# Kernel optimization log

Hardware: AMD Instinct MI355X
Metric: run time of the kernel (lower is better)

The kernel has to match this reference:

```python
import jax, jax.numpy as jnp
import numpy as np

NUM_HEADS = 16
QKV_FEATURES = 2048
HEAD_DIM = QKV_FEATURES // NUM_HEADS
THETA = 10000.0


def compute_freqs_cis(dim, length, start_pos=0, theta=THETA, dtype=jnp.float32):
    freqs = 1.0 / theta ** (jnp.arange(0, dim, 2, dtype=jnp.float32) / dim)
    t = jnp.arange(length, dtype=jnp.float32) + start_pos
    freqs = jnp.outer(t, freqs)  # (L, dim//2)
    return jnp.sin(freqs).astype(dtype), jnp.cos(freqs).astype(dtype)


def apply_rotary_emb(x, sin, cos):
    # x: (B, L, H, D); sin/cos: (L, D//2); interleaved-pair rotation
    x1 = x[..., 0::2]
    x2 = x[..., 1::2]
    sin = sin[None, :, None, :]
    cos = cos[None, :, None, :]
    y1 = x1 * cos - x2 * sin
    y2 = x1 * sin + x2 * cos
    return jnp.stack([y1, y2], axis=-1).reshape(x.shape)


def setup_inputs() -> dict:
    key = jax.random.key(0)
    ks = jax.random.split(key, 6)
    B, L, E = 2, 2048, 2048
    s_in = 1.0 / np.sqrt(E)
    s_out = 1.0 / np.sqrt(QKV_FEATURES)
    return {
        "x": jax.random.normal(ks[0], (B, L, E), jnp.float32),
        "Wq": jax.random.normal(ks[1], (E, QKV_FEATURES), jnp.float32) * s_in,
        "Wk": jax.random.normal(ks[2], (E, QKV_FEATURES), jnp.float32) * s_in,
        "Wv": jax.random.normal(ks[3], (E, QKV_FEATURES), jnp.float32) * s_in,
        "Wo": jax.random.normal(ks[4], (QKV_FEATURES, E), jnp.float32) * s_out,
        "bo": jnp.zeros((E,), jnp.float32),
    }


def reference(x, Wq, Wk, Wv, Wo, bo):
    B, L, E = x.shape
    H, D = NUM_HEADS, HEAD_DIM

    q = (x @ Wq).reshape(B, L, H, D)
    k = (x @ Wk).reshape(B, L, H, D)
    v = (x @ Wv).reshape(B, L, H, D)

    sin, cos = compute_freqs_cis(D, L)
    q = apply_rotary_emb(q, sin, cos)
    k = apply_rotary_emb(k, sin, cos)

    scale = D ** (-0.5)
    sim = jnp.einsum("bqhd,bkhd->bhqk", q, k) * scale

    pos = jnp.arange(L)
    causal_mask = pos[None, :] <= pos[:, None]  # (Lq, Lk)
    sim = jnp.where(causal_mask[None, None, :, :], sim, -1e9)

    attn = jax.nn.softmax(sim, axis=-1)
    out = jnp.einsum("bhqk,bkhd->bqhd", attn, v).reshape(B, L, H * D)
    return out @ Wo + bo
```

## Files before the change

kernel.cpp:

```cpp
#include <hip/hip_runtime.h>
#include <hip/hip_bf16.h>
#include <stdint.h>
#include <stddef.h>

#define B_   2
#define L_   2048
#define E_   2048
#define H_   16
#define D_   128
#define F_   2048
#define NROW (B_*L_)
#define QS   6144

typedef __bf16 bf16_t;
typedef __bf16 bf16x4 __attribute__((ext_vector_type(4)));
typedef __bf16 bf16x8 __attribute__((ext_vector_type(8)));
typedef float  f32x4  __attribute__((ext_vector_type(4)));

__device__ __forceinline__ void gload16(const void* g, void* l) {
  __builtin_amdgcn_global_load_lds(
      (const __attribute__((address_space(1))) void*)g,
      (__attribute__((address_space(3))) void*)l, 16, 0, 0);
}

#define VMC(n)  asm volatile("s_waitcnt vmcnt(" #n ")" ::: "memory")

__global__ __launch_bounds__(256) void k_convert(const float* __restrict__ in,
                                                 bf16_t* __restrict__ out, int n4) {
  int i = blockIdx.x*256 + threadIdx.x;
  if (i >= n4) return;
  float4 v = ((const float4*)in)[i];
  bf16x4 t;
  t[0] = (__bf16)v.x; t[1] = (__bf16)v.y; t[2] = (__bf16)v.z; t[3] = (__bf16)v.w;
  ((bf16x4*)out)[i] = t;
}

__global__ __launch_bounds__(256) void k_transpose_w4(const float* __restrict__ Wq,
                                                      const float* __restrict__ Wk,
                                                      const float* __restrict__ Wv,
                                                      const float* __restrict__ Wo,
                                                      bf16_t* __restrict__ wqkvt,
                                                      bf16_t* __restrict__ wot) {
  __shared__ float tile[32][33];
  const int z = blockIdx.z;
  const float* in = (z == 0) ? Wq : (z == 1) ? Wk : (z == 2) ? Wv : Wo;
  bf16_t* out = (z < 3) ? wqkvt + (size_t)z*F_*E_ : wot;
  const int ct = blockIdx.x, rt = blockIdx.y;
  const int c = threadIdx.x & 31, r0 = threadIdx.x >> 5;
  #pragma unroll
  for (int k = 0; k < 4; k++) {
    int r = r0 + k*8;
    tile[r][c] = in[(size_t)(rt*32 + r)*2048 + ct*32 + c];
  }
  __syncthreads();
  #pragma unroll
  for (int k = 0; k < 4; k++) {
    int r = r0 + k*8;
    out[(size_t)(ct*32 + r)*2048 + rt*32 + c] = (__bf16)tile[c][r];
  }
}

__global__ __launch_bounds__(256) void k_sincos(float2* __restrict__ sc) {
  int id = blockIdx.x*256 + threadIdx.x;
  int t = id >> 6, i = id & 63;
  float freq = powf(10000.0f, -(float)i / 64.0f);
  float a = (float)t * freq;
  sc[id] = make_float2(cosf(a), sinf(a));
}

__global__ __launch_bounds__(256) void k_rope2(bf16_t* __restrict__ qkv,
                                               const float2* __restrict__ sc,
                                               float qscale, int half) {
  int i = blockIdx.x*256 + threadIdx.x;
  const int part = (i >= half);
  int j = part ? i - half : i;
  int e  = j << 2;
  int d  = e & (F_-1);
  int ii = (d & (D_-1)) >> 1;
  int r  = e >> 11;
  int t  = r & (L_-1);
  bf16_t* p = qkv + (size_t)r*QS + part*F_ + d;
  const float scale = part ? 1.0f : qscale;
  bf16x4 v = *(const bf16x4*)p;
  float2 cs0 = sc[t*64 + ii];
  float2 cs1 = sc[t*64 + ii + 1];
  cs0.x *= scale; cs0.y *= scale; cs1.x *= scale; cs1.y *= scale;
  float x0 = (float)v[0], x1 = (float)v[1], x2 = (float)v[2], x3 = (float)v[3];
  bf16x4 o;
  o[0] = (__bf16)(x0*cs0.x - x1*cs0.y);
  o[1] = (__bf16)(x0*cs0.y + x1*cs0.x);
  o[2] = (__bf16)(x2*cs1.x - x3*cs1.y);
  o[3] = (__bf16)(x2*cs1.y + x3*cs1.x);
  *(bf16x4*)p = o;
}

__global__ __launch_bounds__(256) void k_transpose_v(const bf16_t* __restrict__ in,
                                                     bf16_t* __restrict__ out) {
  __shared__ bf16_t tile[32][33];
  const int lt = blockIdx.x, dt = blockIdx.y, bh = blockIdx.z;
  const int b = bh >> 4;
  const int h = bh & 15;
  const int c = threadIdx.x & 31, r0 = threadIdx.x >> 5;
  #pragma unroll
  for (int k = 0; k < 4; k++) {
    int r = r0 + k*8;
    tile[r][c] = in[(size_t)(b*L_ + lt*32 + r)*QS + h*D_ + dt*32 + c];
  }
  __syncthreads();
  #pragma unroll
  for (int k = 0; k < 4; k++) {
    int r = r0 + k*8;
    out[(size_t)(bh*D_ + dt*32 + r)*L_ + lt*32 + c] = tile[c][r];
  }
}

template<typename OutT, bool BIAS>
__global__ __launch_bounds__(256, 3) void k_gemm_bt(const bf16_t* __restrict__ A,
                                                    const bf16_t* __restrict__ BT,
                                                    OutT* __restrict__ C,
                                                    const float* __restrict__ bias,
                                                    int M, int N, int K) {
  __shared__ char sm[49152];
  const int tid = threadIdx.x, lane = tid & 63, wave = tid >> 6;
  const int wr = wave >> 1, wc = wave & 1;
  const int lr = lane & 15, lg = lane >> 4;
  const int nbx = N >> 7, nwg = nbx * (M >> 7);
  int bid = blockIdx.x;
  const int cpx = nwg >> 3;
  bid = (bid & 7)*cpx + (bid >> 3);
  const int bx = bid % nbx, by = bid / nbx;
  const int row0 = by << 7, col0 = bx << 7;
  const int sr  = tid >> 2;
  const int sxe = (((tid & 3) ^ ((sr >> 1) & 3)) << 3);
  const bf16_t* Ag = A  + (size_t)(row0 + sr)*K + sxe;
  const bf16_t* Bg = BT + (size_t)(col0 + sr)*K + sxe;
  const int dst0 = wave*1024;
  auto stage = [&](int t) {
    char* base = sm + (t % 3)*16384;
    const bf16_t* a = Ag + t*32;
    const bf16_t* b = Bg + t*32;
    gload16(a,                base + dst0);
    gload16(a + (size_t)64*K, base + 4096  + dst0);
    gload16(b,                base + 8192  + dst0);
    gload16(b + (size_t)64*K, base + 12288 + dst0);
  };
  const int cs   = (lg ^ ((lr >> 1) & 3)) << 4;
  const int arow = (wr*64 + lr)*64;
  const int brow = 8192 + (wc*64 + lr)*64;
  f32x4 acc[4][4] = {};
  stage(0); stage(1);
  const int nt = K >> 5;
  for (int t = 0; t < nt; t++) {
    if (t + 2 < nt)      { stage(t + 2); VMC(8); }
    else if (t + 1 < nt) { VMC(4); }
    else                 { VMC(0); }
    __builtin_amdgcn_s_barrier();
    const char* base = sm + (t % 3)*16384;
    bf16x8 af[4], bb[4];
    #pragma unroll
    for (int m = 0; m < 4; m++) af[m] = *(const bf16x8*)(base + arow + m*1024 + cs);
    #pragma unroll
    for (int n = 0; n < 4; n++) bb[n] = *(const bf16x8*)(base + brow + n*1024 + cs);
    asm volatile("s_waitcnt lgkmcnt(0)" ::: "memory");
    __builtin_amdgcn_sched_barrier(0);
    __builtin_amdgcn_s_setprio(1);
    #pragma unroll
    for (int m = 0; m < 4; m++)
      #pragma unroll
      for (int n = 0; n < 4; n++)
        acc[m][n] = __builtin_amdgcn_mfma_f32_16x16x32_bf16(af[m], bb[n], acc[m][n], 0, 0, 0);
    __builtin_amdgcn_s_setprio(0);
    __builtin_amdgcn_s_barrier();
  }
  #pragma unroll
  for (int m = 0; m < 4; m++) {
    #pragma unroll
    for (int n = 0; n < 4; n++) {
      const int col = col0 + wc*64 + n*16 + lr;
      const float bv = BIAS ? bias[col] : 0.0f;
      #pragma unroll
      for (int j = 0; j < 4; j++) {
        const int row = row0 + wr*64 + m*16 + lg*4 + j;
        C[(size_t)row*N + col] = (OutT)(acc[m][n][j] + bv);
      }
    }
  }
}

template<bool MASK>
__device__ __forceinline__ void attn_tile(
    int kv0, int wq0, int lr, int lg,
    const char* __restrict__ Kb, const char* __restrict__ Vb, char* __restrict__ Pb,
    const bf16x8 (&aq)[4], f32x4 (&o)[8], float& mrow, float& lsum) {
  const int swz = (lr & 7) << 4;
  f32x4 s[4] = {};
  #pragma unroll
  for (int kd = 0; kd < 4; kd++) {
    bf16x8 ak[4];
    #pragma unroll
    for (int n = 0; n < 4; n++)
      ak[n] = *(const bf16x8*)(Kb + (n*16 + lr)*256 + (((kd*4 + lg) << 4) ^ swz));
    __builtin_amdgcn_s_setprio(1);
    #pragma unroll
    for (int n = 0; n < 4; n++)
      s[n] = __builtin_amdgcn_mfma_f32_16x16x32_bf16(ak[n], aq[kd], s[n], 0, 0, 0);
    __builtin_amdgcn_s_setprio(0);
  }
  if (MASK) {
    const int q = wq0 + lr;
    #pragma unroll
    for (int n = 0; n < 4; n++)
      #pragma unroll
      for (int j = 0; j < 4; j++)
        if (kv0 + n*16 + lg*4 + j > q) s[n][j] = -30000.0f;
  }
  float pmax = fmaxf(
      fmaxf(fmaxf(fmaxf(s[0][0], s[0][1]), fmaxf(s[0][2], s[0][3])),
            fmaxf(fmaxf(s[1][0], s[1][1]), fmaxf(s[1][2], s[1][3]))),
      fmaxf(fmaxf(fmaxf(s[2][0], s[2][1]), fmaxf(s[2][2], s[2][3])),
            fmaxf(fmaxf(s[3][0], s[3][1]), fmaxf(s[3][2], s[3][3]))));
  pmax = fmaxf(pmax, __shfl_xor(pmax, 16));
  pmax = fmaxf(pmax, __shfl_xor(pmax, 32));
  if (!__all(pmax - mrow <= 8.0f)) {
    const float mnew = fmaxf(mrow, pmax);
    const float corr = exp2f(mrow - mnew);
    mrow = mnew;
    lsum *= corr;
    #pragma unroll
    for (int n2 = 0; n2 < 8; n2++) o[n2] *= corr;
  }
  float rs = 0.0f;
  #pragma unroll
  for (int n = 0; n < 4; n++)
    #pragma unroll
    for (int j = 0; j < 4; j++) {
      float p = exp2f(s[n][j] - mrow);
      s[n][j] = p;
      rs += p;
    }
  rs += __shfl_xor(rs, 16);
  rs += __shfl_xor(rs, 32);
  lsum += rs;
  #pragma unroll
  for (int n = 0; n < 4; n++) {
    bf16x4 pw;
    pw[0] = (__bf16)s[n][0]; pw[1] = (__bf16)s[n][1];
    pw[2] = (__bf16)s[n][2]; pw[3] = (__bf16)s[n][3];
    *(bf16x4*)(Pb + ((lr*128 + n*32 + lg*8) ^ swz)) = pw;
  }
  #pragma unroll
  for (int ks = 0; ks < 2; ks++) {
    bf16x8 pb = *(const bf16x8*)(Pb + ((lr*128 + ks*64 + lg*16) ^ swz));
    __builtin_amdgcn_s_setprio(1);
    #pragma unroll
    for (int n2 = 0; n2 < 8; n2++) {
      bf16x8 av = *(const bf16x8*)(Vb + (n2*16 + lr)*128 + (((ks*4 + lg) << 4) ^ swz));
      o[n2] = __builtin_amdgcn_mfma_f32_16x16x32_bf16(av, pb, o[n2], 0, 0, 0);
    }
    __builtin_amdgcn_s_setprio(0);
  }
}

__global__ __launch_bounds__(512, 4) void k_attn(const bf16_t* __restrict__ QKV,
                                                 const bf16_t* __restrict__ Vt,
                                                 bf16_t* __restrict__ O) {
  __shared__ bf16_t Ks[2][64*128];
  __shared__ bf16_t Vs[2][128*64];
  __shared__ bf16_t Pl[8][16*64];
  const int tid = threadIdx.x, lane = tid & 63, wave = tid >> 6;
  const int qt = (int)gridDim.x - 1 - (int)blockIdx.x;
  const int h = blockIdx.y, b = blockIdx.z;
  const int wq0 = qt*128 + wave*16;
  const int lr = lane & 15, lg = lane >> 4;
  char* Pb = (char*)&Pl[wave][0];
  const bf16_t* Q = QKV;
  const bf16_t* K = QKV + F_;

  bf16x8 aq[4];
  #pragma unroll
  for (int kd = 0; kd < 4; kd++)
    aq[kd] = *(const bf16x8*)&Q[(size_t)(b*L_ + wq0 + lr)*QS + h*D_ + kd*32 + lg*8];

  const int kr = tid >> 4, kc = tid & 15;
  const bf16_t* Kg0 = K + (size_t)(b*L_ + kr)*QS + h*D_ + ((kc ^ (kr & 7)) << 3);
  const int vr = tid >> 3, vc = tid & 7;
  const bf16_t* Vg0 = Vt + (size_t)((b*H_ + h)*D_ + vr)*L_ + ((vc ^ (vr & 7)) << 3);

  f32x4 o[8] = {};
  float mrow = -3.0e38f, lsum = 0.0f;
  const int ntb   = 2*qt + 2;
  const int nfull = (wq0 + 1) >> 6;
  const int nmine = ((wq0 + 15) >> 6) + 1;

  {
    char* kb = (char*)&Ks[0][0] + wave*1024;
    char* vb = (char*)&Vs[0][0] + wave*1024;
    gload16(Kg0,                 kb);
    gload16(Kg0 + (size_t)32*QS, kb + 8192);
    gload16(Vg0,                 vb);
    gload16(Vg0 + (size_t)64*L_, vb + 8192);
  }
  __syncthreads();

  int buf = 0;
  for (int t = 0; t < ntb; t++) {
    if (t + 1 < ntb) {
      const int kn = (t+1)*64;
      char* kb = (char*)&Ks[buf^1][0] + wave*1024;
      char* vb = (char*)&Vs[buf^1][0] + wave*1024;
      const bf16_t* kg = Kg0 + (size_t)kn*QS;
      const bf16_t* vg = Vg0 + kn;
      gload16(kg,                 kb);
      gload16(kg + (size_t)32*QS, kb + 8192);
      gload16(vg,                 vb);
      gload16(vg + (size_t)64*L_, vb + 8192);
    }
    const char* Kb = (const char*)&Ks[buf][0];
    const char* Vb = (const char*)&Vs[buf][0];
    if (t < nfull)
      attn_tile<false>(t*64, wq0, lr, lg, Kb, Vb, Pb, aq, o, mrow, lsum);
    else if (t < nmine)
      attn_tile<true >(t*64, wq0, lr, lg, Kb, Vb, Pb, aq, o, mrow, lsum);
    __syncthreads();
    buf ^= 1;
  }
  const float inv = 1.0f / lsum;
  bf16_t* orow = O + (size_t)(b*L_ + wq0 + lr)*F_ + h*D_ + lg*4;
  #pragma unroll
  for (int n2 = 0; n2 < 8; n2++) {
    bf16x4 ov;
    ov[0] = (__bf16)(o[n2][0]*inv); ov[1] = (__bf16)(o[n2][1]*inv);
    ov[2] = (__bf16)(o[n2][2]*inv); ov[3] = (__bf16)(o[n2][3]*inv);
    *(bf16x4*)(orow + n2*16) = ov;
  }
}

extern "C" void kernel_launch(void* const* d_in, const int* in_sizes, int n_in,
                              void* d_out, int out_size, void* d_ws, size_t ws_size,
                              hipStream_t stream) {
  const float* x  = (const float*)d_in[0];
  const float* Wq = (const float*)d_in[1];
  const float* Wk = (const float*)d_in[2];
  const float* Wv = (const float*)d_in[3];
  const float* Wo = (const float*)d_in[4];
  const float* bo = (const float*)d_in[5];
  float* out = (float*)d_out;

  char* ws = (char*)d_ws;
  size_t off = 0;
  auto alloc = [&](size_t bytes) {
    char* p = ws + off;
    off = (off + bytes + 255) & ~(size_t)255;
    return p;
  };
  bf16_t* xb    = (bf16_t*)alloc((size_t)NROW*E_*2);
  bf16_t* wqkvt = (bf16_t*)alloc((size_t)3*F_*E_*2);
  bf16_t* wot   = (bf16_t*)alloc((size_t)F_*E_*2);
  float2* sc    = (float2*)alloc((size_t)L_*64*sizeof(float2));
  bf16_t* qkv   = (bf16_t*)alloc((size_t)NROW*QS*2);
  bf16_t* vt    = (bf16_t*)alloc((size_t)NROW*F_*2);
  bf16_t* ob    = xb;

  const float scale2 = 0.08838834764831845f * 1.44269504088896f;

  k_convert<<<dim3((NROW*E_/4 + 255)/256), 256, 0, stream>>>(x, xb, NROW*E_/4);
  k_transpose_w4<<<dim3(64, 64, 4), 256, 0, stream>>>(Wq, Wk, Wv, Wo, wqkvt, wot);
  k_sincos<<<dim3(L_*64/256), 256, 0, stream>>>(sc);

  k_gemm_bt<bf16_t, false><<<dim3((QS/128)*(NROW/128)), 256, 0, stream>>>(
      xb, wqkvt, qkv, nullptr, NROW, QS, E_);

  k_rope2<<<dim3(2*(NROW*F_/4)/256), 256, 0, stream>>>(qkv, sc, scale2, NROW*F_/4);
  k_transpose_v<<<dim3(L_/32, D_/32, B_*H_), 256, 0, stream>>>(qkv + 2*F_, vt);

  k_attn<<<dim3(L_/128, H_, B_), 512, 0, stream>>>(qkv, vt, ob);

  k_gemm_bt<float, true><<<dim3((E_/128)*(NROW/128)), 256, 0, stream>>>(
      ob, wot, out, bo, NROW, E_, F_);
}
```

Baseline: 443.3 us.

## Add 256x256 QKV GEMM, merge prep/rope kernels, remap attention and GEMM grids

Replaces the 128x128 QKV projection GEMM with a new 512-thread 256x256 tile kernel using double-buffered LDS and interleaved load/MFMA phases, to raise data reuse per tile. Merges the convert/transpose/sincos launches into one prep kernel and the rope/V-transpose launches into one kernel, cutting launch count. Remaps the attention and output-GEMM block indices so blocks sharing a head or column band land on the same XCD. The big tile uses 128KB LDS and one block per CU, which lowers occupancy and leaves fewer, larger blocks.

```diff
diff --git a/kernel.cpp b/kernel.cpp
--- a/kernel.cpp
+++ b/kernel.cpp
@@ -24,93 +24,199 @@
 }
 
 #define VMC(n)  asm volatile("s_waitcnt vmcnt(" #n ")" ::: "memory")
-
-__global__ __launch_bounds__(256) void k_convert(const float* __restrict__ in,
-                                                 bf16_t* __restrict__ out, int n4) {
-  int i = blockIdx.x*256 + threadIdx.x;
-  if (i >= n4) return;
-  float4 v = ((const float4*)in)[i];
-  bf16x4 t;
-  t[0] = (__bf16)v.x; t[1] = (__bf16)v.y; t[2] = (__bf16)v.z; t[3] = (__bf16)v.w;
-  ((bf16x4*)out)[i] = t;
-}
-
-__global__ __launch_bounds__(256) void k_transpose_w4(const float* __restrict__ Wq,
-                                                      const float* __restrict__ Wk,
-                                                      const float* __restrict__ Wv,
-                                                      const float* __restrict__ Wo,
-                                                      bf16_t* __restrict__ wqkvt,
-                                                      bf16_t* __restrict__ wot) {
-  __shared__ float tile[32][33];
-  const int z = blockIdx.z;
-  const float* in = (z == 0) ? Wq : (z == 1) ? Wk : (z == 2) ? Wv : Wo;
-  bf16_t* out = (z < 3) ? wqkvt + (size_t)z*F_*E_ : wot;
-  const int ct = blockIdx.x, rt = blockIdx.y;
-  const int c = threadIdx.x & 31, r0 = threadIdx.x >> 5;
-  #pragma unroll
-  for (int k = 0; k < 4; k++) {
-    int r = r0 + k*8;
-    tile[r][c] = in[(size_t)(rt*32 + r)*2048 + ct*32 + c];
-  }
-  __syncthreads();
-  #pragma unroll
-  for (int k = 0; k < 4; k++) {
-    int r = r0 + k*8;
-    out[(size_t)(ct*32 + r)*2048 + rt*32 + c] = (__bf16)tile[c][r];
-  }
-}
-
-__global__ __launch_bounds__(256) void k_sincos(float2* __restrict__ sc) {
-  int id = blockIdx.x*256 + threadIdx.x;
-  int t = id >> 6, i = id & 63;
-  float freq = powf(10000.0f, -(float)i / 64.0f);
-  float a = (float)t * freq;
-  sc[id] = make_float2(cosf(a), sinf(a));
-}
-
-__global__ __launch_bounds__(256) void k_rope2(bf16_t* __restrict__ qkv,
-                                               const float2* __restrict__ sc,
-                                               float qscale, int half) {
-  int i = blockIdx.x*256 + threadIdx.x;
-  const int part = (i >= half);
-  int j = part ? i - half : i;
-  int e  = j << 2;
-  int d  = e & (F_-1);
-  int ii = (d & (D_-1)) >> 1;
-  int r  = e >> 11;
-  int t  = r & (L_-1);
-  bf16_t* p = qkv + (size_t)r*QS + part*F_ + d;
-  const float scale = part ? 1.0f : qscale;
-  bf16x4 v = *(const bf16x4*)p;
-  float2 cs0 = sc[t*64 + ii];
-  float2 cs1 = sc[t*64 + ii + 1];
-  cs0.x *= scale; cs0.y *= scale; cs1.x *= scale; cs1.y *= scale;
-  float x0 = (float)v[0], x1 = (float)v[1], x2 = (float)v[2], x3 = (float)v[3];
-  bf16x4 o;
-  o[0] = (__bf16)(x0*cs0.x - x1*cs0.y);
-  o[1] = (__bf16)(x0*cs0.y + x1*cs0.x);
-  o[2] = (__bf16)(x2*cs1.x - x3*cs1.y);
-  o[3] = (__bf16)(x2*cs1.y + x3*cs1.x);
-  *(bf16x4*)p = o;
-}
-
-__global__ __launch_bounds__(256) void k_transpose_v(const bf16_t* __restrict__ in,
-                                                     bf16_t* __restrict__ out) {
-  __shared__ bf16_t tile[32][33];
-  const int lt = blockIdx.x, dt = blockIdx.y, bh = blockIdx.z;
-  const int b = bh >> 4;
-  const int h = bh & 15;
-  const int c = threadIdx.x & 31, r0 = threadIdx.x >> 5;
-  #pragma unroll
-  for (int k = 0; k < 4; k++) {
-    int r = r0 + k*8;
-    tile[r][c] = in[(size_t)(b*L_ + lt*32 + r)*QS + h*D_ + dt*32 + c];
-  }
-  __syncthreads();
-  #pragma unroll
-  for (int k = 0; k < 4; k++) {
-    int r = r0 + k*8;
-    out[(size_t)(bh*D_ + dt*32 + r)*L_ + lt*32 + c] = tile[c][r];
+#define BAR_MID do { asm volatile("" ::: "memory"); __builtin_amdgcn_s_barrier(); \
+  asm volatile("s_waitcnt lgkmcnt(0)" ::: "memory"); __builtin_amdgcn_sched_barrier(0); } while(0)
+#define BAR_END do { asm volatile("" ::: "memory"); __builtin_amdgcn_s_barrier(); } while(0)
+
+__global__ __launch_bounds__(256) void k_prep(const float* __restrict__ x,
+                                              const float* __restrict__ Wq,
+                                              const float* __restrict__ Wk,
+                                              const float* __restrict__ Wv,
+                                              const float* __restrict__ Wo,
+                                              bf16_t* __restrict__ xb,
+                                              bf16_t* __restrict__ wqkvt,
+                                              bf16_t* __restrict__ wot,
+                                              float2* __restrict__ sc) {
+  const int bb = blockIdx.x;
+  if (bb < 8192) {
+    int i = bb*256 + threadIdx.x;
+    float4 v = ((const float4*)x)[i];
+    bf16x4 t;
+    t[0] = (__bf16)v.x; t[1] = (__bf16)v.y; t[2] = (__bf16)v.z; t[3] = (__bf16)v.w;
+    ((bf16x4*)xb)[i] = t;
+  } else if (bb < 24576) {
+    __shared__ float tile[32][33];
+    const int r4 = bb - 8192;
+    const int z  = r4 >> 12;
+    const int xy = r4 & 4095;
+    const int ct = xy & 63, rt = xy >> 6;
+    const float* in = (z == 0) ? Wq : (z == 1) ? Wk : (z == 2) ? Wv : Wo;
+    bf16_t* out = (z < 3) ? wqkvt + (size_t)z*F_*E_ : wot;
+    const int c = threadIdx.x & 31, r0 = threadIdx.x >> 5;
+    #pragma unroll
+    for (int k = 0; k < 4; k++) {
+      int r = r0 + k*8;
+      tile[r][c] = in[(size_t)(rt*32 + r)*2048 + ct*32 + c];
+    }
+    __syncthreads();
+    #pragma unroll
+    for (int k = 0; k < 4; k++) {
+      int r = r0 + k*8;
+      out[(size_t)(ct*32 + r)*2048 + rt*32 + c] = (__bf16)tile[c][r];
+    }
+  } else {
+    int id = (bb - 24576)*256 + threadIdx.x;
+    int t = id >> 6, i = id & 63;
+    float freq = powf(10000.0f, -(float)i / 64.0f);
+    float a = (float)t * freq;
+    sc[id] = make_float2(cosf(a), sinf(a));
+  }
+}
+
+__global__ __launch_bounds__(256) void k_ropetv(bf16_t* __restrict__ qkv,
+                                                bf16_t* __restrict__ vt,
+                                                const float2* __restrict__ sc,
+                                                float qscale) {
+  const int bb = blockIdx.x;
+  if (bb < 16384) {
+    const int half = NROW*F_/4;
+    int i = bb*256 + threadIdx.x;
+    const int part = (i >= half);
+    int j = part ? i - half : i;
+    int e  = j << 2;
+    int d  = e & (F_-1);
+    int ii = (d & (D_-1)) >> 1;
+    int r  = e >> 11;
+    int t  = r & (L_-1);
+    bf16_t* p = qkv + (size_t)r*QS + part*F_ + d;
+    const float scale = part ? 1.0f : qscale;
+    bf16x4 v = *(const bf16x4*)p;
+    float2 cs0 = sc[t*64 + ii];
+    float2 cs1 = sc[t*64 + ii + 1];
+    cs0.x *= scale; cs0.y *= scale; cs1.x *= scale; cs1.y *= scale;
+    float x0 = (float)v[0], x1 = (float)v[1], x2 = (float)v[2], x3 = (float)v[3];
+    bf16x4 o;
+    o[0] = (__bf16)(x0*cs0.x - x1*cs0.y);
+    o[1] = (__bf16)(x0*cs0.y + x1*cs0.x);
+    o[2] = (__bf16)(x2*cs1.x - x3*cs1.y);
+    o[3] = (__bf16)(x2*cs1.y + x3*cs1.x);
+    *(bf16x4*)p = o;
+  } else {
+    __shared__ bf16_t tile[32][33];
+    const int r8 = bb - 16384;
+    const int lt = r8 & 63, dt = (r8 >> 6) & 3, bh = r8 >> 8;
+    const int b = bh >> 4, h = bh & 15;
+    const int c = threadIdx.x & 31, r0 = threadIdx.x >> 5;
+    #pragma unroll
+    for (int k = 0; k < 4; k++) {
+      int r = r0 + k*8;
+      tile[r][c] = qkv[(size_t)(b*L_ + lt*32 + r)*QS + 2*F_ + h*D_ + dt*32 + c];
+    }
+    __syncthreads();
+    #pragma unroll
+    for (int k = 0; k < 4; k++) {
+      int r = r0 + k*8;
+      vt[(size_t)(bh*D_ + dt*32 + r)*L_ + lt*32 + c] = tile[c][r];
+    }
+  }
+}
+
+#define RDA03(BASE) do { _Pragma("unroll") for (int m_=0;m_<4;m_++) { \
+  a[m_][0] = *(const bf16x8*)((BASE) + m_*2048 + cs0); \
+  a[m_][1] = *(const bf16x8*)((BASE) + m_*2048 + cs1); } } while(0)
+#define RDA47(BASE) do { _Pragma("unroll") for (int m_=0;m_<4;m_++) { \
+  a[m_][0] = *(const bf16x8*)((BASE) + (m_+4)*2048 + cs0); \
+  a[m_][1] = *(const bf16x8*)((BASE) + (m_+4)*2048 + cs1); } } while(0)
+#define RDB01(BASE) do { _Pragma("unroll") for (int n_=0;n_<2;n_++) { \
+  b[n_][0] = *(const bf16x8*)((BASE) + n_*2048 + cs0); \
+  b[n_][1] = *(const bf16x8*)((BASE) + n_*2048 + cs1); } } while(0)
+#define RDB23(BASE) do { _Pragma("unroll") for (int n_=0;n_<2;n_++) { \
+  b[2+n_][0] = *(const bf16x8*)((BASE) + (2+n_)*2048 + cs0); \
+  b[2+n_][1] = *(const bf16x8*)((BASE) + (2+n_)*2048 + cs1); } } while(0)
+#define MM16(MB, NB) do { __builtin_amdgcn_s_setprio(1); \
+  _Pragma("unroll") for (int m_=0;m_<4;m_++) { \
+    _Pragma("unroll") for (int n_=0;n_<2;n_++) { \
+      acc[(MB)+m_][(NB)+n_] = __builtin_amdgcn_mfma_f32_16x16x32_bf16(a[m_][0], b[(NB)+n_][0], acc[(MB)+m_][(NB)+n_], 0, 0, 0); \
+      acc[(MB)+m_][(NB)+n_] = __builtin_amdgcn_mfma_f32_16x16x32_bf16(a[m_][1], b[(NB)+n_][1], acc[(MB)+m_][(NB)+n_], 0, 0, 0); } } \
+  __builtin_amdgcn_s_setprio(0); } while(0)
+
+template<typename OutT, bool BIAS>
+__global__ __launch_bounds__(512, 1) void k_gemm256(const bf16_t* __restrict__ A,
+                                                    const bf16_t* __restrict__ BT,
+                                                    OutT* __restrict__ C,
+                                                    const float* __restrict__ bias,
+                                                    int M, int N, int K) {
+  __shared__ char sm[131072];
+  const int tid = threadIdx.x, lane = tid & 63, wave = tid >> 6;
+  const int wr = wave >> 2, wc = wave & 3;
+  const int lr = lane & 15, lg = lane >> 4;
+  const int nbx = N >> 8;
+  const int band = nbx >> 3;
+  const int bid = blockIdx.x;
+  const int idx = bid >> 3;
+  const int bx = (bid & 7)*band + idx % band;
+  const int by = idx / band;
+  const int row0 = by << 8, col0 = bx << 8;
+  const int sr  = tid >> 3;
+  const int sxe = ((tid & 7) ^ (sr & 7)) << 3;
+  const bf16_t* Ag = A  + (size_t)(row0 + sr)*K + sxe;
+  const bf16_t* Bg = BT + (size_t)(col0 + sr)*K + sxe;
+  char* smA = sm;
+  char* smB = sm + 65536;
+  const int dst0 = wave*1024;
+  auto stA = [&](int buf, int h, int kt) {
+    const bf16_t* s = Ag + (size_t)(h*128)*K + kt;
+    char* d = smA + buf*32768 + h*16384 + dst0;
+    gload16(s, d); gload16(s + (size_t)64*K, d + 8192);
+  };
+  auto stB = [&](int buf, int h, int kt) {
+    const bf16_t* s = Bg + (size_t)(h*128)*K + kt;
+    char* d = smB + buf*32768 + h*16384 + dst0;
+    gload16(s, d); gload16(s + (size_t)64*K, d + 8192);
+  };
+  const int cs0 = (lg ^ (lr & 7)) << 4;
+  const int cs1 = ((4 + lg) ^ (lr & 7)) << 4;
+
+  f32x4 acc[8][4] = {};
+  bf16x8 a[4][2], b[4][2];
+
+  stA(0,0,0); stA(0,1,0); stB(0,0,0); stB(0,1,0);
+  stA(1,0,64); stB(1,0,64); stB(1,1,64);
+  VMC(6);
+  BAR_END;
+
+  const int nt = K >> 6;
+  for (int u = 0; u < nt; u++) {
+    const int buf = u & 1;
+    const char* Ab = smA + buf*32768 + wr*16384 + lr*128;
+    const char* Bb = smB + buf*32768 + (wc >> 1)*16384 + ((wc & 1)*64 + lr)*128;
+    RDA03(Ab); RDB01(Bb);
+    if (u + 1 < nt) stA(buf^1, 1, (u+1) << 6);
+    BAR_MID; MM16(0,0); BAR_END;
+    RDB23(Bb);
+    BAR_MID; MM16(0,2); BAR_END;
+    RDA47(Ab);
+    if (u + 2 < nt) { stB(buf, 0, (u+2) << 6); stB(buf, 1, (u+2) << 6); }
+    BAR_MID; MM16(4,0); BAR_END;
+    if (u + 2 < nt) {
+      stA(buf, 0, (u+2) << 6);
+      BAR_MID; MM16(4,2); VMC(6); BAR_END;
+    } else {
+      BAR_MID; MM16(4,2); VMC(0); BAR_END;
+    }
+  }
+  #pragma unroll
+  for (int m = 0; m < 8; m++) {
+    #pragma unroll
+    for (int n = 0; n < 4; n++) {
+      const int col = col0 + wc*64 + n*16 + lr;
+      const float bv = BIAS ? bias[col] : 0.0f;
+      #pragma unroll
+      for (int j = 0; j < 4; j++) {
+        const int row = row0 + wr*128 + m*16 + lg*4 + j;
+        C[(size_t)row*N + col] = (OutT)(acc[m][n][j] + bv);
+      }
+    }
   }
 }
 
@@ -124,11 +230,12 @@
   const int tid = threadIdx.x, lane = tid & 63, wave = tid >> 6;
   const int wr = wave >> 1, wc = wave & 1;
   const int lr = lane & 15, lg = lane >> 4;
-  const int nbx = N >> 7, nwg = nbx * (M >> 7);
-  int bid = blockIdx.x;
-  const int cpx = nwg >> 3;
-  bid = (bid & 7)*cpx + (bid >> 3);
-  const int bx = bid % nbx, by = bid / nbx;
+  const int nbx = N >> 7;
+  const int band = nbx >> 3;
+  const int bid = blockIdx.x;
+  const int idx = bid >> 3;
+  const int bx = (bid & 7)*band + idx % band;
+  const int by = idx / band;
   const int row0 = by << 7, col0 = bx << 7;
   const int sr  = tid >> 2;
   const int sxe = (((tid & 3) ^ ((sr >> 1) & 3)) << 3);
@@ -268,8 +375,11 @@
   __shared__ bf16_t Vs[2][128*64];
   __shared__ bf16_t Pl[8][16*64];
   const int tid = threadIdx.x, lane = tid & 63, wave = tid >> 6;
-  const int qt = (int)gridDim.x - 1 - (int)blockIdx.x;
-  const int h = blockIdx.y, b = blockIdx.z;
+  const int bidx = blockIdx.x;
+  const int xcd = bidx & 7, idx = bidx >> 3;
+  const int bh  = xcd*4 + (idx & 3);
+  const int qt  = 15 - (idx >> 2);
+  const int b = bh >> 4, h = bh & 15;
   const int wq0 = qt*128 + wave*16;
   const int lr = lane & 15, lg = lane >> 4;
   char* Pb = (char*)&Pl[wave][0];
@@ -363,17 +473,14 @@
 
   const float scale2 = 0.08838834764831845f * 1.44269504088896f;
 
-  k_convert<<<dim3((NROW*E_/4 + 255)/256), 256, 0, stream>>>(x, xb, NROW*E_/4);
-  k_transpose_w4<<<dim3(64, 64, 4), 256, 0, stream>>>(Wq, Wk, Wv, Wo, wqkvt, wot);
-  k_sincos<<<dim3(L_*64/256), 256, 0, stream>>>(sc);
-
-  k_gemm_bt<bf16_t, false><<<dim3((QS/128)*(NROW/128)), 256, 0, stream>>>(
+  k_prep<<<dim3(25088), 256, 0, stream>>>(x, Wq, Wk, Wv, Wo, xb, wqkvt, wot, sc);
+
+  k_gemm256<bf16_t, false><<<dim3((QS/256)*(NROW/256)), 512, 0, stream>>>(
       xb, wqkvt, qkv, nullptr, NROW, QS, E_);
 
-  k_rope2<<<dim3(2*(NROW*F_/4)/256), 256, 0, stream>>>(qkv, sc, scale2, NROW*F_/4);
-  k_transpose_v<<<dim3(L_/32, D_/32, B_*H_), 256, 0, stream>>>(qkv + 2*F_, vt);
-
-  k_attn<<<dim3(L_/128, H_, B_), 512, 0, stream>>>(qkv, vt, ob);
+  k_ropetv<<<dim3(24576), 256, 0, stream>>>(qkv, vt, sc, scale2);
+
+  k_attn<<<dim3(512), 512, 0, stream>>>(qkv, vt, ob);
 
   k_gemm_bt<float, true><<<dim3((E_/128)*(NROW/128)), 256, 0, stream>>>(
       ob, wot, out, bo, NROW, E_, F_);
```

Result: faster. 402.2 us (-9.3%).
